# Optimization experiments

Measured on AMD Instinct MI355X. Metric: run time of the kernel, lower is better.

## Reference

```python
import jax, jax.numpy as jnp
import numpy as np

N = 8192      # num nodes
D = 256       # input feature dim (num_embeddings)
F_OUT = 128   # out_channels
B = 4096      # lookup batch size


def setup_inputs() -> dict:
    key = jax.random.key(0)
    k1, k2, k3, k4 = jax.random.split(key, 4)
    x = jax.random.randint(k1, (B,), 0, N)                      # node ids for final lookup
    adj = jax.random.randint(k2, (N, N), 0, 2).astype(jnp.int32)  # dense 0/1 adjacency
    embedding = jax.random.normal(k3, (N, D), dtype=jnp.float32)
    xavier = 1.414 * (6.0 / (D + F_OUT)) ** 0.5
    W = jax.random.uniform(k4, (D, F_OUT), minval=-xavier, maxval=xavier, dtype=jnp.float32)
    return {"x": x, "adj": adj, "embedding": embedding, "W": W}


def reference(x, adj, embedding, W):
    Wh = embedding @ W                                   # [N, F_OUT]
    mask = adj > 0
    maskf = mask.astype(Wh.dtype)
    # per-row neighbor mean of Wh (vectorized form of the python row loop)
    deg = jnp.maximum(jnp.sum(maskf, axis=1), 1.0)       # guard; random adj has deg>0
    neigh_mean = (maskf @ Wh) / deg[:, None]             # [N, F_OUT]
    alpha = jnp.sum(Wh * neigh_mean, axis=1)             # [N], Wh[i] . mean(neighbors)
    e = Wh @ Wh.T + alpha[:, None]                       # similarity + row-wise query term
    att = jax.nn.softmax(jnp.where(mask, e, jnp.asarray(-9e15, e.dtype)), axis=1)
    # dropout is identity in eval mode (p effectively 0)
    h_prime = att @ Wh                                   # [N, F_OUT]
    emb_out = jax.nn.elu(h_prime)                        # concat=True branch
    out = emb_out[x]                                     # F.embedding lookup, [B, F_OUT]
    nrm = jnp.linalg.norm(out, axis=1, keepdims=True)
    return out / jnp.maximum(nrm, 1e-12)                 # F.normalize (L2, eps=1e-12)
```

## Files before the change

kernel.cpp:

```cpp
#include <hip/hip_runtime.h>

#define NN 8192
#define DD 256
#define FF 128
#define BB 4096
#define NSPLIT 16
#define KCHUNK (NN / NSPLIT)
#define NITER (KCHUNK / 64)

typedef unsigned short ushortT;
typedef _Float16 f16;
typedef __attribute__((ext_vector_type(8))) _Float16 f16x8;
typedef __attribute__((ext_vector_type(4))) float f32x4;

__device__ __forceinline__ ushortT f2h_bits(float f) {
  f16 h = (f16)f; ushortT u; __builtin_memcpy(&u, &h, 2); return u;
}
__device__ __forceinline__ float h_bits2f(ushortT u) {
  f16 h; __builtin_memcpy(&h, &u, 2); return (float)h;
}


__global__ __launch_bounds__(256) void init_kernel(int* flags, int* cnt) {
  int i = blockIdx.x * 256 + threadIdx.x;
  flags[i] = 0;
  if (i == 0) *cnt = 0;
}

__global__ __launch_bounds__(256) void scatter_kernel(const int* __restrict__ x, int* flags) {
  int b = blockIdx.x * 256 + threadIdx.x;
  flags[x[b]] = 1;
}

__global__ __launch_bounds__(256) void compact_kernel(const int* __restrict__ flags, int* cnt,
                                                      int* list, int* slot) {
  int i = blockIdx.x * 256 + threadIdx.x;
  if (flags[i]) {
    int pos = atomicAdd(cnt, 1);
    list[pos] = i;
    slot[i] = pos;
  }
}


__global__ __launch_bounds__(256) void pack_kernel(const int* __restrict__ adj,
                                                   const int* __restrict__ list,
                                                   const int* __restrict__ cntp,
                                                   unsigned* __restrict__ pk) {
  const int s = blockIdx.x >> 2;
  const int kc = (blockIdx.x & 3) * 2048;
  if (s >= *cntp) return;
  const int w = threadIdx.x >> 6, l = threadIdx.x & 63;
  const int* base = adj + (size_t)list[s] * NN + kc + w * 512;
  unsigned long long* dst = (unsigned long long*)(pk + s * 256 + (kc >> 5) + w * 16);
#pragma unroll
  for (int i = 0; i < 8; ++i) {
    unsigned long long b = __ballot(base[i * 64 + l] > 0);
    if (l == 0) dst[i] = b;
  }
}


__global__ __launch_bounds__(256) void wh_kernel(const float* __restrict__ emb,
                                                 const float* __restrict__ W,
                                                 ushortT* __restrict__ Whh,
                                                 ushortT* __restrict__ Whl) {
  __shared__ float Es[32 * 65];
  __shared__ float Ws[64 * 128];
  const int t = threadIdx.x;
  const int r0 = blockIdx.x * 32;
  const int rg = t >> 5;
  const int cg = t & 31;
  float4 acc[4] = {{0,0,0,0},{0,0,0,0},{0,0,0,0},{0,0,0,0}};
  for (int kc = 0; kc < DD; kc += 64) {
    __syncthreads();
    for (int i = 0; i < 8; ++i) {
      int idx = t + 256 * i;
      int r = idx >> 6, k = idx & 63;
      Es[r * 65 + k] = emb[(r0 + r) * DD + kc + k];
    }
    for (int i = 0; i < 8; ++i) {
      int idx = t + 256 * i;
      int kr = idx >> 5, c4 = (idx & 31) * 4;
      *(float4*)&Ws[kr * 128 + c4] = *(const float4*)&W[(kc + kr) * 128 + c4];
    }
    __syncthreads();
    for (int k = 0; k < 64; ++k) {
      float4 b = *(const float4*)&Ws[k * 128 + cg * 4];
#pragma unroll
      for (int i = 0; i < 4; ++i) {
        float a = Es[(rg * 4 + i) * 65 + k];
        acc[i].x += a * b.x; acc[i].y += a * b.y;
        acc[i].z += a * b.z; acc[i].w += a * b.w;
      }
    }
  }
#pragma unroll
  for (int i = 0; i < 4; ++i) {
    int row = r0 + rg * 4 + i;
    float v[4] = {acc[i].x, acc[i].y, acc[i].z, acc[i].w};
    ushort4 hh, ll;
    ushortT* hp = (ushortT*)&hh;
    ushortT* lp = (ushortT*)&ll;
#pragma unroll
    for (int k = 0; k < 4; ++k) {
      ushortT h = f2h_bits(v[k]);
      hp[k] = h;
      lp[k] = f2h_bits(v[k] - h_bits2f(h));
    }
    *(ushort4*)&Whh[row * FF + cg * 4] = hh;
    *(ushort4*)&Whl[row * FF + cg * 4] = ll;
  }
}


__global__ __launch_bounds__(256) void transpose_kernel(const ushortT* __restrict__ A,
                                                        ushortT* __restrict__ At) {
  __shared__ ushortT tile[64 * 72];
  const int t = threadIdx.x;
  const int r0 = (blockIdx.x >> 1) * 64, c0 = (blockIdx.x & 1) * 64;
#pragma unroll
  for (int i = 0; i < 2; ++i) {
    int idx = t + 256 * i;
    int r = idx >> 3, cb = idx & 7;
    *(ushort4*)&tile[r * 72 + ((cb ^ ((r >> 3) & 7)) * 8)] =
        *(const ushort4*)&A[(size_t)(r0 + r) * FF + c0 + cb * 8];
    *(ushort4*)&tile[r * 72 + ((cb ^ ((r >> 3) & 7)) * 8) + 4] =
        *(const ushort4*)&A[(size_t)(r0 + r) * FF + c0 + cb * 8 + 4];
  }
  __syncthreads();
#pragma unroll
  for (int i = 0; i < 2; ++i) {
    int idx = t + 256 * i;
    int f = idx >> 3, r8 = idx & 7;
    ushortT v[8];
#pragma unroll
    for (int u = 0; u < 8; ++u) {
      int row = r8 * 8 + u;
      v[u] = tile[row * 72 + (((f >> 3) ^ ((row >> 3) & 7)) * 8) + (f & 7)];
    }
    *(ushort4*)&At[(size_t)(c0 + f) * NN + r0 + r8 * 8] = *(ushort4*)&v[0];
    *(ushort4*)&At[(size_t)(c0 + f) * NN + r0 + r8 * 8 + 4] = *(ushort4*)&v[4];
  }
}


__global__ __launch_bounds__(256, 3) void attn_kernel(
    const ushortT* __restrict__ Whh, const ushortT* __restrict__ Whl,
    const ushortT* __restrict__ WhT, const unsigned* __restrict__ pk,
    const int* __restrict__ list, const int* __restrict__ cntp,
    float* __restrict__ Opart, float* __restrict__ mpart, float* __restrict__ lpart) {
  __shared__ short Kh[2][64 * 128];
  __shared__ short Ps[4][16 * 72];
  __shared__ int nid[64];

  const int cnt = *cntp;
  const int qblk = blockIdx.x >> 4, chunk = blockIdx.x & 15;
  const int q0 = qblk * 64;
  if (q0 >= cnt) return;

  const int t = threadIdx.x;
  if (t < 64) nid[t] = list[min(q0 + t, cnt - 1)];
  const int kt0 = chunk * KCHUNK;

  f16x8 sg[4];
#pragma unroll
  for (int i = 0; i < 4; ++i) {
    int idx = t + 256 * i;
    sg[i] = *(const f16x8*)(Whh + (size_t)(kt0 + (idx >> 4)) * FF + (idx & 15) * 8);
  }
  __syncthreads();
#pragma unroll
  for (int i = 0; i < 4; ++i) {
    int idx = t + 256 * i;
    int r = idx >> 4, cb = idx & 15;
    *(f16x8*)&Kh[0][r * 128 + ((cb ^ (r & 7)) * 8)] = sg[i];
  }

  const int w = t >> 6, l = t & 63, quad = l >> 4, c = l & 15;

  const size_t qr = (size_t)nid[w * 16 + c] * FF;
  f16x8 qh[4], ql[4];
#pragma unroll
  for (int ks = 0; ks < 4; ++ks) {
    qh[ks] = *(const f16x8*)(Whh + qr + ks * 32 + quad * 8);
    ql[ks] = *(const f16x8*)(Whl + qr + ks * 32 + quad * 8);
  }
  int prow[4];
#pragma unroll
  for (int r = 0; r < 4; ++r) prow[r] = min(q0 + w * 16 + quad * 4 + r, cnt - 1);

  float m[4], lr[4];
#pragma unroll
  for (int r = 0; r < 4; ++r) { m[r] = -1e30f; lr[r] = 0.f; }
  f32x4 O[8] = {{0,0,0,0},{0,0,0,0},{0,0,0,0},{0,0,0,0},
                {0,0,0,0},{0,0,0,0},{0,0,0,0},{0,0,0,0}};

  for (int it = 0; it < NITER; ++it) {
    const int kt = kt0 + it * 64;
    const int cur = it & 1;
    unsigned mw0[4], mw1[4];
#pragma unroll
    for (int r = 0; r < 4; ++r) {
      uint2 mm = *(const uint2*)(pk + (size_t)prow[r] * 256 + (kt >> 5));
      mw0[r] = mm.x; mw1[r] = mm.y;
    }
    if (it + 1 < NITER) {
#pragma unroll
      for (int i = 0; i < 4; ++i) {
        int idx = t + 256 * i;
        sg[i] = *(const f16x8*)(Whh + (size_t)(kt + 64 + (idx >> 4)) * FF + (idx & 15) * 8);
      }
    }
    __syncthreads();
    if (it + 1 < NITER) {
#pragma unroll
      for (int i = 0; i < 4; ++i) {
        int idx = t + 256 * i;
        int r = idx >> 4, cb = idx & 15;
        *(f16x8*)&Kh[1 - cur][r * 128 + ((cb ^ (r & 7)) * 8)] = sg[i];
      }
    }

    f32x4 sacc[4];
#pragma unroll
    for (int nt = 0; nt < 4; ++nt) {
      const int rb = (nt * 16 + c) * 128;
      f32x4 a = {0, 0, 0, 0};
#pragma unroll
      for (int ks = 0; ks < 4; ++ks) {
        const int off = rb + (((ks * 4 + quad) ^ (c & 7)) * 8);
        f16x8 kv = *(const f16x8*)&Kh[cur][off];
        a = __builtin_amdgcn_mfma_f32_16x16x32_f16(qh[ks], kv, a, 0, 0, 0);
        a = __builtin_amdgcn_mfma_f32_16x16x32_f16(ql[ks], kv, a, 0, 0, 0);
      }
      sacc[nt] = a;
    }

    float rmax[4];
#pragma unroll
    for (int r = 0; r < 4; ++r) {
      float v = -1e30f;
#pragma unroll
      for (int nt = 0; nt < 4; ++nt) {
        unsigned bit = ((nt < 2 ? mw0[r] : mw1[r]) >> ((nt & 1) * 16 + c)) & 1u;
        v = fmaxf(v, bit ? sacc[nt][r] : -1e30f);
      }
      rmax[r] = v;
    }
#pragma unroll
    for (int mk = 1; mk <= 8; mk <<= 1)
#pragma unroll
      for (int r = 0; r < 4; ++r) rmax[r] = fmaxf(rmax[r], __shfl_xor(rmax[r], mk, 16));
    float sc[4], psum[4];
#pragma unroll
    for (int r = 0; r < 4; ++r) {
      float nm = fmaxf(m[r], rmax[r]);
      sc[r] = __expf(m[r] - nm);
      m[r] = nm;
      psum[r] = 0.f;
    }
#pragma unroll
    for (int nt = 0; nt < 4; ++nt)
#pragma unroll
      for (int r = 0; r < 4; ++r) {
        unsigned bit = ((nt < 2 ? mw0[r] : mw1[r]) >> ((nt & 1) * 16 + c)) & 1u;
        float p = bit ? __expf(sacc[nt][r] - m[r]) : 0.f;
        ushortT pb = f2h_bits(p);
        Ps[w][(quad * 4 + r) * 72 + nt * 16 + c] = (short)pb;
        psum[r] += h_bits2f(pb);
      }
#pragma unroll
    for (int mk = 1; mk <= 8; mk <<= 1)
#pragma unroll
      for (int r = 0; r < 4; ++r) psum[r] += __shfl_xor(psum[r], mk, 16);
#pragma unroll
    for (int r = 0; r < 4; ++r) lr[r] = lr[r] * sc[r] + psum[r];

#pragma unroll
    for (int ft = 0; ft < 8; ++ft)
#pragma unroll
      for (int r = 0; r < 4; ++r) O[ft][r] *= sc[r];
    f16x8 pa[2];
#pragma unroll
    for (int ks2 = 0; ks2 < 2; ++ks2)
      pa[ks2] = *(const f16x8*)&Ps[w][c * 72 + ks2 * 32 + quad * 8];
#pragma unroll
    for (int ft = 0; ft < 8; ++ft) {
      const ushortT* vp = WhT + (size_t)(ft * 16 + c) * NN + kt + quad * 8;
#pragma unroll
      for (int ks2 = 0; ks2 < 2; ++ks2) {
        f16x8 vb = *(const f16x8*)(vp + ks2 * 32);
        O[ft] = __builtin_amdgcn_mfma_f32_16x16x32_f16(pa[ks2], vb, O[ft], 0, 0, 0);
      }
    }
  }

  float* Op = Opart + (size_t)chunk * 4096 * FF;
#pragma unroll
  for (int ft = 0; ft < 8; ++ft)
#pragma unroll
    for (int r = 0; r < 4; ++r)
      Op[(size_t)(q0 + w * 16 + quad * 4 + r) * FF + ft * 16 + c] = O[ft][r];
  if (c == 0) {
#pragma unroll
    for (int r = 0; r < 4; ++r) {
      mpart[chunk * 4096 + q0 + w * 16 + quad * 4 + r] = m[r];
      lpart[chunk * 4096 + q0 + w * 16 + quad * 4 + r] = lr[r];
    }
  }
}


__global__ __launch_bounds__(128) void combine_kernel(
    const float* __restrict__ Opart, const float* __restrict__ mpart,
    const float* __restrict__ lpart, float* __restrict__ h) {
  const int r = blockIdx.x;
  const int t = threadIdx.x;
  float mstar = -1e30f;
#pragma unroll
  for (int c = 0; c < NSPLIT; ++c) mstar = fmaxf(mstar, mpart[c * 4096 + r]);
  float lstar = 0.f, acc = 0.f;
#pragma unroll
  for (int c = 0; c < NSPLIT; ++c) {
    float wgt = __expf(mpart[c * 4096 + r] - mstar);
    lstar += wgt * lpart[c * 4096 + r];
    acc += wgt * Opart[((size_t)c * 4096 + r) * FF + t];
  }
  float v = acc / fmaxf(lstar, 1e-30f);
  h[r * FF + t] = v > 0.f ? v : expm1f(v);
}


__global__ __launch_bounds__(128) void out_kernel(const int* __restrict__ x,
                                                  const int* __restrict__ slot,
                                                  const float* __restrict__ h,
                                                  float* __restrict__ out) {
  const int b = blockIdx.x, t = threadIdx.x;
  const int s = slot[x[b]];
  float v = h[s * FF + t];
  float ss = v * v;
#pragma unroll
  for (int wd = 1; wd <= 32; wd <<= 1) ss += __shfl_xor(ss, wd);
  __shared__ float red[2];
  if ((t & 63) == 0) red[t >> 6] = ss;
  __syncthreads();
  float tot = red[0] + red[1];
  float scale = 1.f / fmaxf(sqrtf(tot), 1e-12f);
  out[b * FF + t] = v * scale;
}


extern "C" void kernel_launch(void* const* d_in, const int* in_sizes, int n_in,
                              void* d_out, int out_size, void* d_ws, size_t ws_size,
                              hipStream_t stream) {
  const int*   x   = (const int*)d_in[0];
  const int*   adj = (const int*)d_in[1];
  const float* emb = (const float*)d_in[2];
  const float* W   = (const float*)d_in[3];
  float* out = (float*)d_out;

  char* base = (char*)d_ws;
  ushortT* Whh = (ushortT*)(base);
  ushortT* Whl = (ushortT*)(base + 2097152);
  float*   h   = (float*)(base + 2097152);
  ushortT* WhT = (ushortT*)(base + 4194304);
  float* Opart = (float*)(base + 6291456);
  float* mpart = (float*)(base + 39845888);
  float* lpart = (float*)(base + 40108032);
  unsigned* pk = (unsigned*)(base + 40370176);
  int*   flags = (int*)(base + 44564480);
  int*   list  = (int*)(base + 44597248);
  int*   slot  = (int*)(base + 44613632);
  int*   cnt   = (int*)(base + 44646400);
  (void)in_sizes; (void)n_in; (void)out_size; (void)ws_size;

  hipLaunchKernelGGL(init_kernel,      dim3(NN / 256), dim3(256), 0, stream, flags, cnt);
  hipLaunchKernelGGL(scatter_kernel,   dim3(BB / 256), dim3(256), 0, stream, x, flags);
  hipLaunchKernelGGL(compact_kernel,   dim3(NN / 256), dim3(256), 0, stream, flags, cnt, list, slot);
  hipLaunchKernelGGL(pack_kernel,      dim3(4096 * 4), dim3(256), 0, stream, adj, list, cnt, pk);
  hipLaunchKernelGGL(wh_kernel,        dim3(NN / 32),  dim3(256), 0, stream, emb, W, Whh, Whl);
  hipLaunchKernelGGL(transpose_kernel, dim3((NN / 64) * 2), dim3(256), 0, stream, Whh, WhT);
  hipLaunchKernelGGL(attn_kernel,      dim3((BB / 64) * NSPLIT), dim3(256), 0, stream,
                     Whh, Whl, WhT, pk, list, cnt, Opart, mpart, lpart);
  hipLaunchKernelGGL(combine_kernel,   dim3(4096), dim3(128), 0, stream, Opart, mpart, lpart, h);
  hipLaunchKernelGGL(out_kernel,       dim3(BB),   dim3(128), 0, stream, x, slot, h, out);
}
```

Measured before the change: 475.3 us.

## Fuse dedup, transpose and combine stages; use exp2 with prescaled queries

Replaces the three dedup kernels with a single-block shared-memory dedup kernel. Folds the Wh transpose into wh_kernel's epilogue and merges combine with the output normalisation. Prescales queries by log2(e) so the softmax can use exp2f, and moves the adjacency bitmask loads after the prefetch barrier. This cuts launches and intermediate traffic, at the cost of a serial single-block dedup and uncoalesced strided WhT stores.

```diff
diff --git a/kernel.cpp b/kernel.cpp
--- a/kernel.cpp
+++ b/kernel.cpp
@@ -21,25 +21,26 @@
 }
 
 
-__global__ __launch_bounds__(256) void init_kernel(int* flags, int* cnt) {
-  int i = blockIdx.x * 256 + threadIdx.x;
-  flags[i] = 0;
-  if (i == 0) *cnt = 0;
-}
-
-__global__ __launch_bounds__(256) void scatter_kernel(const int* __restrict__ x, int* flags) {
-  int b = blockIdx.x * 256 + threadIdx.x;
-  flags[x[b]] = 1;
-}
-
-__global__ __launch_bounds__(256) void compact_kernel(const int* __restrict__ flags, int* cnt,
-                                                      int* list, int* slot) {
-  int i = blockIdx.x * 256 + threadIdx.x;
-  if (flags[i]) {
-    int pos = atomicAdd(cnt, 1);
-    list[pos] = i;
-    slot[i] = pos;
-  }
+__global__ __launch_bounds__(1024) void dedup_kernel(const int* __restrict__ x,
+                                                     int* __restrict__ list,
+                                                     int* __restrict__ slot,
+                                                     int* __restrict__ cnt) {
+  __shared__ int flags[NN];
+  __shared__ int lcnt;
+  const int t = threadIdx.x;
+  for (int i = t; i < NN; i += 1024) flags[i] = 0;
+  if (t == 0) lcnt = 0;
+  __syncthreads();
+  for (int i = t; i < BB; i += 1024) flags[x[i]] = 1;
+  __syncthreads();
+  for (int i = t; i < NN; i += 1024)
+    if (flags[i]) {
+      int pos = atomicAdd(&lcnt, 1);
+      list[pos] = i;
+      slot[i] = pos;
+    }
+  __syncthreads();
+  if (t == 0) *cnt = lcnt;
 }
 
 
@@ -64,7 +65,8 @@
 __global__ __launch_bounds__(256) void wh_kernel(const float* __restrict__ emb,
                                                  const float* __restrict__ W,
                                                  ushortT* __restrict__ Whh,
-                                                 ushortT* __restrict__ Whl) {
+                                                 ushortT* __restrict__ Whl,
+                                                 ushortT* __restrict__ WhT) {
   __shared__ float Es[32 * 65];
   __shared__ float Ws[64 * 128];
   const int t = threadIdx.x;
@@ -95,6 +97,7 @@
       }
     }
   }
+  ushortT hv[4][4];
 #pragma unroll
   for (int i = 0; i < 4; ++i) {
     int row = r0 + rg * 4 + i;
@@ -107,41 +110,14 @@
       ushortT h = f2h_bits(v[k]);
       hp[k] = h;
       lp[k] = f2h_bits(v[k] - h_bits2f(h));
+      hv[k][i] = h;
     }
     *(ushort4*)&Whh[row * FF + cg * 4] = hh;
     *(ushort4*)&Whl[row * FF + cg * 4] = ll;
   }
-}
-
-
-__global__ __launch_bounds__(256) void transpose_kernel(const ushortT* __restrict__ A,
-                                                        ushortT* __restrict__ At) {
-  __shared__ ushortT tile[64 * 72];
-  const int t = threadIdx.x;
-  const int r0 = (blockIdx.x >> 1) * 64, c0 = (blockIdx.x & 1) * 64;
-#pragma unroll
-  for (int i = 0; i < 2; ++i) {
-    int idx = t + 256 * i;
-    int r = idx >> 3, cb = idx & 7;
-    *(ushort4*)&tile[r * 72 + ((cb ^ ((r >> 3) & 7)) * 8)] =
-        *(const ushort4*)&A[(size_t)(r0 + r) * FF + c0 + cb * 8];
-    *(ushort4*)&tile[r * 72 + ((cb ^ ((r >> 3) & 7)) * 8) + 4] =
-        *(const ushort4*)&A[(size_t)(r0 + r) * FF + c0 + cb * 8 + 4];
-  }
-  __syncthreads();
-#pragma unroll
-  for (int i = 0; i < 2; ++i) {
-    int idx = t + 256 * i;
-    int f = idx >> 3, r8 = idx & 7;
-    ushortT v[8];
-#pragma unroll
-    for (int u = 0; u < 8; ++u) {
-      int row = r8 * 8 + u;
-      v[u] = tile[row * 72 + (((f >> 3) ^ ((row >> 3) & 7)) * 8) + (f & 7)];
-    }
-    *(ushort4*)&At[(size_t)(c0 + f) * NN + r0 + r8 * 8] = *(ushort4*)&v[0];
-    *(ushort4*)&At[(size_t)(c0 + f) * NN + r0 + r8 * 8 + 4] = *(ushort4*)&v[4];
-  }
+#pragma unroll
+  for (int k = 0; k < 4; ++k)
+    *(ushort4*)&WhT[(size_t)(cg * 4 + k) * NN + r0 + rg * 4] = *(ushort4*)&hv[k][0];
 }
 
 
@@ -183,8 +159,15 @@
   f16x8 qh[4], ql[4];
 #pragma unroll
   for (int ks = 0; ks < 4; ++ks) {
-    qh[ks] = *(const f16x8*)(Whh + qr + ks * 32 + quad * 8);
-    ql[ks] = *(const f16x8*)(Whl + qr + ks * 32 + quad * 8);
+    f16x8 h8 = *(const f16x8*)(Whh + qr + ks * 32 + quad * 8);
+    f16x8 l8 = *(const f16x8*)(Whl + qr + ks * 32 + quad * 8);
+#pragma unroll
+    for (int u = 0; u < 8; ++u) {
+      float q = ((float)h8[u] + (float)l8[u]) * 1.4426950408889634f;
+      f16 hi = (f16)q;
+      qh[ks][u] = hi;
+      ql[ks][u] = (f16)(q - (float)hi);
+    }
   }
   int prow[4];
 #pragma unroll
@@ -199,12 +182,6 @@
   for (int it = 0; it < NITER; ++it) {
     const int kt = kt0 + it * 64;
     const int cur = it & 1;
-    unsigned mw0[4], mw1[4];
-#pragma unroll
-    for (int r = 0; r < 4; ++r) {
-      uint2 mm = *(const uint2*)(pk + (size_t)prow[r] * 256 + (kt >> 5));
-      mw0[r] = mm.x; mw1[r] = mm.y;
-    }
     if (it + 1 < NITER) {
 #pragma unroll
       for (int i = 0; i < 4; ++i) {
@@ -220,6 +197,12 @@
         int r = idx >> 4, cb = idx & 15;
         *(f16x8*)&Kh[1 - cur][r * 128 + ((cb ^ (r & 7)) * 8)] = sg[i];
       }
+    }
+    unsigned mw0[4], mw1[4];
+#pragma unroll
+    for (int r = 0; r < 4; ++r) {
+      uint2 mm = *(const uint2*)(pk + (size_t)prow[r] * 256 + (kt >> 5));
+      mw0[r] = mm.x; mw1[r] = mm.y;
     }
 
     f32x4 sacc[4];
@@ -256,7 +239,7 @@
 #pragma unroll
     for (int r = 0; r < 4; ++r) {
       float nm = fmaxf(m[r], rmax[r]);
-      sc[r] = __expf(m[r] - nm);
+      sc[r] = exp2f(m[r] - nm);
       m[r] = nm;
       psum[r] = 0.f;
     }
@@ -265,7 +248,7 @@
 #pragma unroll
       for (int r = 0; r < 4; ++r) {
         unsigned bit = ((nt < 2 ? mw0[r] : mw1[r]) >> ((nt & 1) * 16 + c)) & 1u;
-        float p = bit ? __expf(sacc[nt][r] - m[r]) : 0.f;
+        float p = bit ? exp2f(sacc[nt][r] - m[r]) : 0.f;
         ushortT pb = f2h_bits(p);
         Ps[w][(quad * 4 + r) * 72 + nt * 16 + c] = (short)pb;
         psum[r] += h_bits2f(pb);
@@ -312,33 +295,24 @@
 }
 
 
-__global__ __launch_bounds__(128) void combine_kernel(
+__global__ __launch_bounds__(128) void combine_out(
+    const int* __restrict__ x, const int* __restrict__ slot,
     const float* __restrict__ Opart, const float* __restrict__ mpart,
-    const float* __restrict__ lpart, float* __restrict__ h) {
-  const int r = blockIdx.x;
-  const int t = threadIdx.x;
-  float mstar = -1e30f;
-#pragma unroll
-  for (int c = 0; c < NSPLIT; ++c) mstar = fmaxf(mstar, mpart[c * 4096 + r]);
-  float lstar = 0.f, acc = 0.f;
-#pragma unroll
-  for (int c = 0; c < NSPLIT; ++c) {
-    float wgt = __expf(mpart[c * 4096 + r] - mstar);
-    lstar += wgt * lpart[c * 4096 + r];
-    acc += wgt * Opart[((size_t)c * 4096 + r) * FF + t];
-  }
-  float v = acc / fmaxf(lstar, 1e-30f);
-  h[r * FF + t] = v > 0.f ? v : expm1f(v);
-}
-
-
-__global__ __launch_bounds__(128) void out_kernel(const int* __restrict__ x,
-                                                  const int* __restrict__ slot,
-                                                  const float* __restrict__ h,
-                                                  float* __restrict__ out) {
+    const float* __restrict__ lpart, float* __restrict__ out) {
   const int b = blockIdx.x, t = threadIdx.x;
   const int s = slot[x[b]];
-  float v = h[s * FF + t];
+  float mstar = -1e30f;
+#pragma unroll
+  for (int c = 0; c < NSPLIT; ++c) mstar = fmaxf(mstar, mpart[c * 4096 + s]);
+  float lstar = 0.f, acc = 0.f;
+#pragma unroll
+  for (int c = 0; c < NSPLIT; ++c) {
+    float wgt = exp2f(mpart[c * 4096 + s] - mstar);
+    lstar += wgt * lpart[c * 4096 + s];
+    acc += wgt * Opart[((size_t)c * 4096 + s) * FF + t];
+  }
+  float v = acc / fmaxf(lstar, 1e-30f);
+  v = v > 0.f ? v : expm1f(v);
   float ss = v * v;
 #pragma unroll
   for (int wd = 1; wd <= 32; wd <<= 1) ss += __shfl_xor(ss, wd);
@@ -363,26 +337,21 @@
   char* base = (char*)d_ws;
   ushortT* Whh = (ushortT*)(base);
   ushortT* Whl = (ushortT*)(base + 2097152);
-  float*   h   = (float*)(base + 2097152);
   ushortT* WhT = (ushortT*)(base + 4194304);
   float* Opart = (float*)(base + 6291456);
   float* mpart = (float*)(base + 39845888);
   float* lpart = (float*)(base + 40108032);
   unsigned* pk = (unsigned*)(base + 40370176);
-  int*   flags = (int*)(base + 44564480);
-  int*   list  = (int*)(base + 44597248);
-  int*   slot  = (int*)(base + 44613632);
-  int*   cnt   = (int*)(base + 44646400);
+  int*   list  = (int*)(base + 44564480);
+  int*   slot  = (int*)(base + 44580864);
+  int*   cnt   = (int*)(base + 44613632);
   (void)in_sizes; (void)n_in; (void)out_size; (void)ws_size;
 
-  hipLaunchKernelGGL(init_kernel,      dim3(NN / 256), dim3(256), 0, stream, flags, cnt);
-  hipLaunchKernelGGL(scatter_kernel,   dim3(BB / 256), dim3(256), 0, stream, x, flags);
-  hipLaunchKernelGGL(compact_kernel,   dim3(NN / 256), dim3(256), 0, stream, flags, cnt, list, slot);
-  hipLaunchKernelGGL(pack_kernel,      dim3(4096 * 4), dim3(256), 0, stream, adj, list, cnt, pk);
-  hipLaunchKernelGGL(wh_kernel,        dim3(NN / 32),  dim3(256), 0, stream, emb, W, Whh, Whl);
-  hipLaunchKernelGGL(transpose_kernel, dim3((NN / 64) * 2), dim3(256), 0, stream, Whh, WhT);
-  hipLaunchKernelGGL(attn_kernel,      dim3((BB / 64) * NSPLIT), dim3(256), 0, stream,
+  hipLaunchKernelGGL(dedup_kernel, dim3(1),        dim3(1024), 0, stream, x, list, slot, cnt);
+  hipLaunchKernelGGL(pack_kernel,  dim3(4096 * 4), dim3(256),  0, stream, adj, list, cnt, pk);
+  hipLaunchKernelGGL(wh_kernel,    dim3(NN / 32),  dim3(256),  0, stream, emb, W, Whh, Whl, WhT);
+  hipLaunchKernelGGL(attn_kernel,  dim3((BB / 64) * NSPLIT), dim3(256), 0, stream,
                      Whh, Whl, WhT, pk, list, cnt, Opart, mpart, lpart);
-  hipLaunchKernelGGL(combine_kernel,   dim3(4096), dim3(128), 0, stream, Opart, mpart, lpart, h);
-  hipLaunchKernelGGL(out_kernel,       dim3(BB),   dim3(128), 0, stream, x, slot, h, out);
-}
+  hipLaunchKernelGGL(combine_out,  dim3(BB), dim3(128), 0, stream,
+                     x, slot, Opart, mpart, lpart, out);
+}
```

Result: no change. 468.3 us (-1.5%).
